# Kernel tuning notes

Hardware: AMD Instinct MI355X
Metric: run time of the kernel (lower is better)

Reference implementation:

```python
import jax, jax.numpy as jnp
import numpy as np

SEQ_LEN, N_VARS, N_SKILLS, D_IN = 120, 9, 32, 1
BATCH = 32768


def setup_inputs() -> dict:
    key = jax.random.key(0)
    ks = jax.random.split(key, 8)
    H, D = N_SKILLS, D_IN
    s = 1.0 / np.sqrt(H)  # torch LSTMCell init scale
    return {
        "x": jax.random.normal(ks[0], (BATCH, N_VARS * SEQ_LEN), dtype=jnp.float32),
        # nn.LSTMCell params (gate order i,f,g,o)
        "W_ih": jax.random.uniform(ks[1], (4 * H, D), jnp.float32, -s, s),
        "W_hh": jax.random.uniform(ks[2], (4 * H, H), jnp.float32, -s, s),
        "b_ih": jax.random.uniform(ks[3], (4 * H,), jnp.float32, -s, s),
        "b_hh": jax.random.uniform(ks[4], (4 * H,), jnp.float32, -s, s),
        # contextual gate params: cg_w Linear(D,H,bias=False), cg_u Linear(H,H)
        "cg_w": jax.random.uniform(ks[5], (H, D), jnp.float32, -s, s),
        "cg_u": jax.random.uniform(ks[6], (H, H), jnp.float32, -s, s),
        "cg_b": jax.random.uniform(ks[7], (H,), jnp.float32, -s, s),
    }


def reference(x, W_ih, W_hh, b_ih, b_hh, cg_w, cg_u, cg_b):
    B = x.shape[0]
    H = N_SKILLS
    # [B, V*T] -> fold the 9 independent variable-sequences into the batch dim
    # (the same cell weights are shared across vars), then scan over time.
    xs = x.reshape(B * N_VARS, SEQ_LEN, D_IN)
    xs = jnp.moveaxis(xs, 1, 0)  # [T, B*V, D_IN]

    def step(carry, xt):
        h, c = carry  # each [B*V, H]
        gates = xt @ W_ih.T + b_ih + h @ W_hh.T + b_hh  # [B*V, 4H]
        i, f, g, o = jnp.split(gates, 4, axis=-1)
        i = jax.nn.sigmoid(i)
        f = jax.nn.sigmoid(f)
        g = jnp.tanh(g)
        c_new = f * c + i * g
        # contextual gate uses the *previous* h
        cg = jax.nn.sigmoid(xt @ cg_w.T + h @ cg_u.T + cg_b)
        h_new = cg * jnp.tanh(c_new)
        return (h_new, c_new), None

    zeros = jnp.zeros((B * N_VARS, H), dtype=x.dtype)
    (h, _), _ = jax.lax.scan(step, (zeros, zeros), xs)
    # [B*V, H] -> [B, V*H] (variable-major, matching torch.cat over vars)
    return h.reshape(B, N_VARS * H)
```

## Files before the change

### kernel.cpp

```cpp
#include <hip/hip_runtime.h>


#define NV 9
#define TLEN 120
#define HS 32
#define BATCH_ 32768
#define NSEQ (BATCH_ * NV)
#define NBATCH (NSEQ / 16)
#define GRID_ 6144

#define XSTRIDE 17
#define HSTRIDE 36

typedef __attribute__((ext_vector_type(8))) short bf16x8;
typedef __attribute__((ext_vector_type(4))) float f32x4;
typedef __attribute__((ext_vector_type(4))) unsigned int u32x4;

__device__ __forceinline__ float fast_exp2(float x) { return __builtin_amdgcn_exp2f(x); }
__device__ __forceinline__ float fast_rcp(float x)  { return __builtin_amdgcn_rcpf(x); }
__device__ __forceinline__ float sigf(float x) {
  return fast_rcp(1.0f + fast_exp2(x * -1.44269504088896f));
}
__device__ __forceinline__ float tanhf_(float x) {
  return fmaf(-2.0f, fast_rcp(1.0f + fast_exp2(x * -2.88539008177793f)), 1.0f);
}
__device__ __forceinline__ unsigned int fbits(float x) { return __builtin_bit_cast(unsigned int, x); }
__device__ __forceinline__ float bcastf(unsigned int x) { return __builtin_bit_cast(float, x); }

__global__ __launch_bounds__(64, 2) void cglstm_kernel(
    const float* __restrict__ x,
    const float* __restrict__ W_ih,
    const float* __restrict__ W_hh,
    const float* __restrict__ b_ih,
    const float* __restrict__ b_hh,
    const float* __restrict__ cg_w,
    const float* __restrict__ cg_u,
    const float* __restrict__ cg_b,
    float* __restrict__ out)
{
  const int lane = threadIdx.x;
  const int col  = lane & 15;
  const int quad = lane >> 4;

  __shared__ float xT[TLEN * XSTRIDE];
  __shared__ unsigned int hbuf[16 * HSTRIDE];

  bf16x8 bhi[8], blo[8];
  float wx[8], bb[8];
#pragma unroll
  for (int tile = 0; tile < 8; ++tile) {
    const int n = col + (tile & 1) * 16;
    const float* wrow = (tile < 6) ? (W_hh + (size_t)((tile >> 1) * HS + n) * HS)
                                   : (cg_u + (size_t)n * HS);
    bf16x8 vh, vl;
#pragma unroll
    for (int e = 0; e < 8; ++e) {
      float wv = wrow[quad * 8 + e];
      unsigned int wbits = fbits(wv);
      float lo_f = wv - bcastf(wbits & 0xffff0000u);
      vh[e] = (short)(wbits >> 16);
      vl[e] = (short)(fbits(lo_f) >> 16);
    }
    bhi[tile] = vh; blo[tile] = vl;
    if (tile < 6) {
      const int gg = tile >> 1;
      wx[tile] = W_ih[gg * HS + n];
      bb[tile] = b_ih[gg * HS + n] + b_hh[gg * HS + n];
    } else {
      wx[tile] = cg_w[n];
      bb[tile] = cg_b[n];
    }
  }

  for (int p = blockIdx.x; p < NBATCH; p += GRID_) {
    const float4* xb = (const float4*)(x + (size_t)p * 16 * TLEN);
    for (int i = lane; i < 480; i += 64) {
      float4 v = xb[i];
      int f0 = i * 4;
      int s  = f0 / TLEN;
      int t0 = f0 - s * TLEN;
      xT[(t0 + 0) * XSTRIDE + s] = v.x;
      xT[(t0 + 1) * XSTRIDE + s] = v.y;
      xT[(t0 + 2) * XSTRIDE + s] = v.z;
      xT[(t0 + 3) * XSTRIDE + s] = v.w;
    }
    for (int i = lane; i < 16 * HSTRIDE; i += 64) hbuf[i] = 0u;
    f32x4 c0 = {0.f, 0.f, 0.f, 0.f}, c1 = c0, h0 = c0, h1 = c0;
    __syncthreads();

#pragma unroll 1
    for (int t = 0; t < TLEN; ++t) {
      float xt0 = xT[t * XSTRIDE + quad * 4 + 0];
      float xt1 = xT[t * XSTRIDE + quad * 4 + 1];
      float xt2 = xT[t * XSTRIDE + quad * 4 + 2];
      float xt3 = xT[t * XSTRIDE + quad * 4 + 3];
      f32x4 acc[8];
#pragma unroll
      for (int tile = 0; tile < 8; ++tile) {
        acc[tile][0] = fmaf(wx[tile], xt0, bb[tile]);
        acc[tile][1] = fmaf(wx[tile], xt1, bb[tile]);
        acc[tile][2] = fmaf(wx[tile], xt2, bb[tile]);
        acc[tile][3] = fmaf(wx[tile], xt3, bb[tile]);
      }
      const unsigned int* hrow = &hbuf[col * HSTRIDE + quad * 8];
      u32x4 wa = *(const u32x4*)hrow;
      u32x4 wz = *(const u32x4*)(hrow + 4);
      u32x4 hi4, lo4;
      hi4[0] = __builtin_amdgcn_perm(wa[1], wa[0], 0x05040100u);
      hi4[1] = __builtin_amdgcn_perm(wa[3], wa[2], 0x05040100u);
      hi4[2] = __builtin_amdgcn_perm(wz[1], wz[0], 0x05040100u);
      hi4[3] = __builtin_amdgcn_perm(wz[3], wz[2], 0x05040100u);
      lo4[0] = __builtin_amdgcn_perm(wa[1], wa[0], 0x07060302u);
      lo4[1] = __builtin_amdgcn_perm(wa[3], wa[2], 0x07060302u);
      lo4[2] = __builtin_amdgcn_perm(wz[1], wz[0], 0x07060302u);
      lo4[3] = __builtin_amdgcn_perm(wz[3], wz[2], 0x07060302u);
      bf16x8 ahi = __builtin_bit_cast(bf16x8, hi4);
      bf16x8 alo = __builtin_bit_cast(bf16x8, lo4);
#pragma unroll
      for (int tile = 0; tile < 8; ++tile) {
        acc[tile] = __builtin_amdgcn_mfma_f32_16x16x32_bf16(ahi, bhi[tile], acc[tile], 0, 0, 0);
        acc[tile] = __builtin_amdgcn_mfma_f32_16x16x32_bf16(alo, bhi[tile], acc[tile], 0, 0, 0);
        acc[tile] = __builtin_amdgcn_mfma_f32_16x16x32_bf16(ahi, blo[tile], acc[tile], 0, 0, 0);
      }
#pragma unroll
      for (int r = 0; r < 4; ++r) {
        float si = sigf(acc[0][r]);
        float sf = sigf(acc[2][r]);
        float tg = tanhf_(acc[4][r]);
        float sc = sigf(acc[6][r]);
        c0[r] = fmaf(sf, c0[r], si * tg);
        float hv = sc * tanhf_(c0[r]);
        h0[r] = hv;
        unsigned int hbits = fbits(hv);
        float lof = hv - bcastf(hbits & 0xffff0000u);
        hbuf[(quad * 4 + r) * HSTRIDE + col] =
            __builtin_amdgcn_perm(fbits(lof), hbits, 0x07060302u);

        float si1 = sigf(acc[1][r]);
        float sf1 = sigf(acc[3][r]);
        float tg1 = tanhf_(acc[5][r]);
        float sc1 = sigf(acc[7][r]);
        c1[r] = fmaf(sf1, c1[r], si1 * tg1);
        float hv1 = sc1 * tanhf_(c1[r]);
        h1[r] = hv1;
        unsigned int hbits1 = fbits(hv1);
        float lof1 = hv1 - bcastf(hbits1 & 0xffff0000u);
        hbuf[(quad * 4 + r) * HSTRIDE + col + 16] =
            __builtin_amdgcn_perm(fbits(lof1), hbits1, 0x07060302u);
      }
      __syncthreads();
    }

    float* ob = out + (size_t)p * 16 * HS;
#pragma unroll
    for (int r = 0; r < 4; ++r) {
      ob[(quad * 4 + r) * HS + col]      = h0[r];
      ob[(quad * 4 + r) * HS + col + 16] = h1[r];
    }
    __syncthreads();
  }
}

extern "C" void kernel_launch(void* const* d_in, const int* in_sizes, int n_in,
                              void* d_out, int out_size, void* d_ws, size_t ws_size,
                              hipStream_t stream) {
  const float* x    = (const float*)d_in[0];
  const float* W_ih = (const float*)d_in[1];
  const float* W_hh = (const float*)d_in[2];
  const float* b_ih = (const float*)d_in[3];
  const float* b_hh = (const float*)d_in[4];
  const float* cg_w = (const float*)d_in[5];
  const float* cg_u = (const float*)d_in[6];
  const float* cg_b = (const float*)d_in[7];
  float* out = (float*)d_out;

  dim3 grid(GRID_), block(64);
  hipLaunchKernelGGL(cglstm_kernel, grid, block, 0, stream,
                     x, W_ih, W_hh, b_ih, b_hh, cg_w, cg_u, cg_b, out);
}
```

Measured before the change: 1.622 ms.

## Fold exp scaling into weights and merge gate reciprocals algebraically

```diff
diff --git a/kernel.cpp b/kernel.cpp
--- a/kernel.cpp
+++ b/kernel.cpp
@@ -9,8 +9,11 @@
 #define NBATCH (NSEQ / 16)
 #define GRID_ 6144
 
-#define XSTRIDE 17
+#define XSTRIDE 20
 #define HSTRIDE 36
+
+#define LOG2E 1.4426950408889634f
+#define TWOL  2.8853900817779268f
 
 typedef __attribute__((ext_vector_type(8))) short bf16x8;
 typedef __attribute__((ext_vector_type(4))) float f32x4;
@@ -18,14 +21,40 @@
 
 __device__ __forceinline__ float fast_exp2(float x) { return __builtin_amdgcn_exp2f(x); }
 __device__ __forceinline__ float fast_rcp(float x)  { return __builtin_amdgcn_rcpf(x); }
-__device__ __forceinline__ float sigf(float x) {
-  return fast_rcp(1.0f + fast_exp2(x * -1.44269504088896f));
-}
-__device__ __forceinline__ float tanhf_(float x) {
-  return fmaf(-2.0f, fast_rcp(1.0f + fast_exp2(x * -2.88539008177793f)), 1.0f);
-}
 __device__ __forceinline__ unsigned int fbits(float x) { return __builtin_bit_cast(unsigned int, x); }
 __device__ __forceinline__ float bcastf(unsigned int x) { return __builtin_bit_cast(float, x); }
+
+__device__ __forceinline__ f32x4 splat4(float x) { f32x4 v = {x, x, x, x}; return v; }
+__device__ __forceinline__ f32x4 fma4(f32x4 a, f32x4 b, f32x4 c) {
+  return __builtin_elementwise_fma(a, b, c);
+}
+__device__ __forceinline__ f32x4 exp24(f32x4 v) {
+  f32x4 r;
+  r[0] = fast_exp2(v[0]); r[1] = fast_exp2(v[1]);
+  r[2] = fast_exp2(v[2]); r[3] = fast_exp2(v[3]);
+  return r;
+}
+__device__ __forceinline__ f32x4 rcp4(f32x4 v) {
+  f32x4 r;
+  r[0] = fast_rcp(v[0]); r[1] = fast_rcp(v[1]);
+  r[2] = fast_rcp(v[2]); r[3] = fast_rcp(v[3]);
+  return r;
+}
+
+__device__ __forceinline__ void lstm_elem(f32x4 ai, f32x4 af, f32x4 ag, f32x4 ac,
+                                          f32x4& ct, f32x4& h) {
+  const f32x4 one4 = splat4(1.0f);
+  f32x4 Ei = exp24(ai), Ef = exp24(af), Eg = exp24(ag), Ea = exp24(ac);
+  f32x4 pi_ = Ei + one4, pf_ = Ef + one4, pg_ = Eg + one4, pa_ = Ea + one4;
+  f32x4 u   = fma4(Eg, splat4(TWOL), splat4(-TWOL));
+  f32x4 P   = pi_ * pg_;
+  f32x4 tt  = pf_ * u;
+  f32x4 num = fma4(ct, P, tt);
+  f32x4 den = pf_ * P;
+  ct = num * rcp4(den);
+  f32x4 Ec  = exp24(ct);
+  h = (one4 - Ec) * rcp4(pa_ * (Ec + one4));
+}
 
 __global__ __launch_bounds__(64, 2) void cglstm_kernel(
     const float* __restrict__ x,
@@ -42,7 +71,7 @@
   const int col  = lane & 15;
   const int quad = lane >> 4;
 
-  __shared__ float xT[TLEN * XSTRIDE];
+  __shared__ __align__(16) float xT[TLEN * XSTRIDE];
   __shared__ unsigned int hbuf[16 * HSTRIDE];
 
   bf16x8 bhi[8], blo[8];
@@ -50,12 +79,13 @@
 #pragma unroll
   for (int tile = 0; tile < 8; ++tile) {
     const int n = col + (tile & 1) * 16;
+    const float sc_ = ((tile >> 1) == 2) ? -TWOL : -LOG2E;
     const float* wrow = (tile < 6) ? (W_hh + (size_t)((tile >> 1) * HS + n) * HS)
                                    : (cg_u + (size_t)n * HS);
     bf16x8 vh, vl;
 #pragma unroll
     for (int e = 0; e < 8; ++e) {
-      float wv = wrow[quad * 8 + e];
+      float wv = wrow[quad * 8 + e] * sc_;
       unsigned int wbits = fbits(wv);
       float lo_f = wv - bcastf(wbits & 0xffff0000u);
       vh[e] = (short)(wbits >> 16);
@@ -64,11 +94,11 @@
     bhi[tile] = vh; blo[tile] = vl;
     if (tile < 6) {
       const int gg = tile >> 1;
-      wx[tile] = W_ih[gg * HS + n];
-      bb[tile] = b_ih[gg * HS + n] + b_hh[gg * HS + n];
+      wx[tile] = W_ih[gg * HS + n] * sc_;
+      bb[tile] = (b_ih[gg * HS + n] + b_hh[gg * HS + n]) * sc_;
     } else {
-      wx[tile] = cg_w[n];
-      bb[tile] = cg_b[n];
+      wx[tile] = cg_w[n] * sc_;
+      bb[tile] = cg_b[n] * sc_;
     }
   }
 
@@ -85,23 +115,16 @@
       xT[(t0 + 3) * XSTRIDE + s] = v.w;
     }
     for (int i = lane; i < 16 * HSTRIDE; i += 64) hbuf[i] = 0u;
-    f32x4 c0 = {0.f, 0.f, 0.f, 0.f}, c1 = c0, h0 = c0, h1 = c0;
+    f32x4 ct0 = splat4(0.f), ct1 = splat4(0.f), h0 = splat4(0.f), h1 = splat4(0.f);
     __syncthreads();
 
 #pragma unroll 1
     for (int t = 0; t < TLEN; ++t) {
-      float xt0 = xT[t * XSTRIDE + quad * 4 + 0];
-      float xt1 = xT[t * XSTRIDE + quad * 4 + 1];
-      float xt2 = xT[t * XSTRIDE + quad * 4 + 2];
-      float xt3 = xT[t * XSTRIDE + quad * 4 + 3];
+      f32x4 xt4 = *(const f32x4*)&xT[t * XSTRIDE + quad * 4];
       f32x4 acc[8];
 #pragma unroll
-      for (int tile = 0; tile < 8; ++tile) {
-        acc[tile][0] = fmaf(wx[tile], xt0, bb[tile]);
-        acc[tile][1] = fmaf(wx[tile], xt1, bb[tile]);
-        acc[tile][2] = fmaf(wx[tile], xt2, bb[tile]);
-        acc[tile][3] = fmaf(wx[tile], xt3, bb[tile]);
-      }
+      for (int tile = 0; tile < 8; ++tile)
+        acc[tile] = fma4(splat4(wx[tile]), xt4, splat4(bb[tile]));
       const unsigned int* hrow = &hbuf[col * HSTRIDE + quad * 8];
       u32x4 wa = *(const u32x4*)hrow;
       u32x4 wz = *(const u32x4*)(hrow + 4);
@@ -122,29 +145,16 @@
         acc[tile] = __builtin_amdgcn_mfma_f32_16x16x32_bf16(alo, bhi[tile], acc[tile], 0, 0, 0);
         acc[tile] = __builtin_amdgcn_mfma_f32_16x16x32_bf16(ahi, blo[tile], acc[tile], 0, 0, 0);
       }
+      lstm_elem(acc[0], acc[2], acc[4], acc[6], ct0, h0);
+      lstm_elem(acc[1], acc[3], acc[5], acc[7], ct1, h1);
 #pragma unroll
       for (int r = 0; r < 4; ++r) {
-        float si = sigf(acc[0][r]);
-        float sf = sigf(acc[2][r]);
-        float tg = tanhf_(acc[4][r]);
-        float sc = sigf(acc[6][r]);
-        c0[r] = fmaf(sf, c0[r], si * tg);
-        float hv = sc * tanhf_(c0[r]);
-        h0[r] = hv;
-        unsigned int hbits = fbits(hv);
-        float lof = hv - bcastf(hbits & 0xffff0000u);
+        unsigned int hbits = fbits(h0[r]);
+        float lof = h0[r] - bcastf(hbits & 0xffff0000u);
         hbuf[(quad * 4 + r) * HSTRIDE + col] =
             __builtin_amdgcn_perm(fbits(lof), hbits, 0x07060302u);
-
-        float si1 = sigf(acc[1][r]);
-        float sf1 = sigf(acc[3][r]);
-        float tg1 = tanhf_(acc[5][r]);
-        float sc1 = sigf(acc[7][r]);
-        c1[r] = fmaf(sf1, c1[r], si1 * tg1);
-        float hv1 = sc1 * tanhf_(c1[r]);
-        h1[r] = hv1;
-        unsigned int hbits1 = fbits(hv1);
-        float lof1 = hv1 - bcastf(hbits1 & 0xffff0000u);
+        unsigned int hbits1 = fbits(h1[r]);
+        float lof1 = h1[r] - bcastf(hbits1 & 0xffff0000u);
         hbuf[(quad * 4 + r) * HSTRIDE + col + 16] =
             __builtin_amdgcn_perm(fbits(lof1), hbits1, 0x07060302u);
       }
```

After: 1.393 ms. -14.1%, faster.
